# Kernel optimization log

Hardware: AMD Instinct MI355X
Metric: run time of the kernel (lower is better)

Reference implementation:

```python
import jax, jax.numpy as jnp
import numpy as np

WIN = (7, 7)
NUM_HEADS = 12
LORA_SCALING = 16.0 / 16.0  # lora_alpha / lora_rank


def _relative_position_index(win):
    wh, ww = win
    coords = np.stack(np.meshgrid(np.arange(wh), np.arange(ww), indexing='ij'))  # (2, wh, ww)
    cf = coords.reshape(2, -1)
    rel = cf[:, :, None] - cf[:, None, :]  # (2, N, N)
    rel = rel.transpose(1, 2, 0)
    rel[:, :, 0] += wh - 1
    rel[:, :, 1] += ww - 1
    rel[:, :, 0] *= 2 * ww - 1
    return jnp.asarray(rel.sum(-1), dtype=jnp.int32)  # (N, N)


def setup_inputs() -> dict:
    key = jax.random.key(0)
    ks = jax.random.split(key, 12)
    B_, N, C, r = 2048, 49, 384, 16
    nW = 64
    s = 0.02
    return {
        'x': jax.random.normal(ks[0], (B_, N, C), jnp.float32),
        'mask': jnp.zeros((nW, N, N), jnp.float32),
        'qkv_w': jax.random.normal(ks[1], (C, 3 * C), jnp.float32) * s,
        'qkv_b': jax.random.normal(ks[2], (3 * C,), jnp.float32) * s,
        'qa_w': jax.random.normal(ks[3], (C, r), jnp.float32) * s,
        'qb_w': jax.random.normal(ks[4], (r, C), jnp.float32) * s,
        'va_w': jax.random.normal(ks[5], (C, r), jnp.float32) * s,
        'vb_w': jax.random.normal(ks[6], (r, C), jnp.float32) * s,
        'rpb_table': jax.random.normal(ks[7], ((2 * WIN[0] - 1) * (2 * WIN[1] - 1), NUM_HEADS), jnp.float32) * s,
        'proj_w': jax.random.normal(ks[8], (C, C), jnp.float32) * s,
        'proj_b': jax.random.normal(ks[9], (C,), jnp.float32) * s,
    }


def reference(x, mask, qkv_w, qkv_b, qa_w, qb_w, va_w, vb_w, rpb_table, proj_w, proj_b):
    B_, N, C = x.shape
    H = NUM_HEADS
    hd = C // H
    scale = hd ** -0.5

    qkv = (x @ qkv_w + qkv_b).reshape(B_, N, 3, H, hd)
    qkv = jnp.transpose(qkv, (2, 0, 3, 1, 4))  # (3, B_, H, N, hd)
    q, k, v = qkv[0], qkv[1], qkv[2]

    q_lora = LORA_SCALING * ((x @ qa_w) @ qb_w)  # (B_, N, C)
    q = q + jnp.transpose(q_lora.reshape(B_, N, H, hd), (0, 2, 1, 3))
    v_lora = LORA_SCALING * ((x @ va_w) @ vb_w)
    v = v + jnp.transpose(v_lora.reshape(B_, N, H, hd), (0, 2, 1, 3))

    attn = jnp.einsum('bhnd,bhmd->bhnm', q * scale, k)  # (B_, H, N, N)

    rel_idx = _relative_position_index(WIN)  # (N, N) static int
    rpb = rpb_table[rel_idx]  # (N, N, H)
    attn = attn + jnp.transpose(rpb, (2, 0, 1))[None]

    nW = mask.shape[0]
    attn = attn.reshape(B_ // nW, nW, H, N, N) + mask[None, :, None]
    attn = attn.reshape(B_, H, N, N)
    attn = jax.nn.softmax(attn, axis=-1)

    out = jnp.einsum('bhnm,bhmd->bhnd', attn, v)
    out = jnp.transpose(out, (0, 2, 1, 3)).reshape(B_, N, C)
    return out @ proj_w + proj_b
```

## Files before the change

kernel.cpp:

```cpp
#include <hip/hip_runtime.h>
#include <hip/hip_bf16.h>

typedef __hip_bfloat16 bf16;
typedef float f32x4 __attribute__((ext_vector_type(4)));
typedef short bf16x8 __attribute__((ext_vector_type(8)));

static __device__ __forceinline__ void gload_lds16(const void* g, void* l) {
    __builtin_amdgcn_global_load_lds(
        (const __attribute__((address_space(1))) void*)g,
        (__attribute__((address_space(3))) void*)l, 16, 0, 0);
}

static __device__ __forceinline__ short bf16bits(float v) {
    bf16 tb = __float2bfloat16(v);
    return *reinterpret_cast<short*>(&tb);
}

__global__ __launch_bounds__(256) void cvt_x_kernel(const float4* __restrict__ x,
                                                    bf16* __restrict__ xb, int n4) {
    int i = blockIdx.x * 256 + threadIdx.x;
    const int stride = gridDim.x * 256;
    for (; i < n4; i += stride) {
        float4 v = x[i];
        alignas(8) bf16 tmp[4];
        tmp[0] = __float2bfloat16(v.x);
        tmp[1] = __float2bfloat16(v.y);
        tmp[2] = __float2bfloat16(v.z);
        tmp[3] = __float2bfloat16(v.w);
        *reinterpret_cast<uint2*>(xb + 4l * i) = *reinterpret_cast<uint2*>(tmp);
    }
}

__global__ __launch_bounds__(256) void build_wefft_kernel(
    const float* __restrict__ qkv_w, const float* __restrict__ qa,
    const float* __restrict__ qb, const float* __restrict__ va,
    const float* __restrict__ vb, bf16* __restrict__ wt) {
    int idx = blockIdx.x * 256 + threadIdx.x;
    int ncol = idx / 384;
    int k = idx - ncol * 384;
    float v = qkv_w[k * 1152 + ncol];
    if (ncol < 384) {
        float s = 0.f;
#pragma unroll
        for (int j = 0; j < 16; ++j) s += qa[k * 16 + j] * qb[j * 384 + ncol];
        v += s;
    } else if (ncol >= 768) {
        int nc = ncol - 768;
        float s = 0.f;
#pragma unroll
        for (int j = 0; j < 16; ++j) s += va[k * 16 + j] * vb[j * 384 + nc];
        v += s;
    }
    wt[(long)ncol * 384 + k] = __float2bfloat16(v);
}

__global__ __launch_bounds__(256) void build_projt_kernel(const float* __restrict__ pw,
                                                          bf16* __restrict__ pt) {
    int idx = blockIdx.x * 256 + threadIdx.x;
    int ncol = idx / 384;
    int k = idx - ncol * 384;
    pt[(long)ncol * 384 + k] = __float2bfloat16(pw[k * 384 + ncol]);
}

__global__ __launch_bounds__(256) void build_cbias_kernel(const float* __restrict__ rpb_table,
                                                          const float* __restrict__ mask,
                                                          float* __restrict__ cbias) {
    int idx = blockIdx.x * 256 + threadIdx.x;
    int hw = idx / 2401;
    int ij = idx - hw * 2401;
    int h = hw >> 6, w = hw & 63;
    int i = ij / 49, j = ij - i * 49;
    int yi = i / 7, xi = i - yi * 7;
    int yj = j / 7, xj = j - yj * 7;
    int rel = (yi - yj + 6) * 13 + (xi - xj + 6);
    cbias[idx] = rpb_table[rel * 12 + h] + mask[w * 2401 + ij];
}

template <bool OUT_BF16>
__global__ __launch_bounds__(256) void gemm_kernel(const bf16* __restrict__ A,
                                                   const bf16* __restrict__ BT,
                                                   const float* __restrict__ bias,
                                                   void* __restrict__ Cout,
                                                   int N, int K, int nxb, int nwg) {
    __shared__ short Al[128 * 64];
    __shared__ short Bl[128 * 64];
    const int t = threadIdx.x;
    const int lane = t & 63;
    const int wave = t >> 6;
    const int wr = wave >> 1;
    const int wc = wave & 1;
    const int g = lane >> 4, c = lane & 15;

    const int q8 = nwg >> 3;
    const int wgid = (blockIdx.x & 7) * q8 + (blockIdx.x >> 3);
    const int by = wgid / nxb;
    const int bx = wgid - by * nxb;
    const long rowBase = (long)by * 128;
    const long colBase = (long)bx * 128;

    f32x4 acc[4][4];
#pragma unroll
    for (int m = 0; m < 4; ++m)
#pragma unroll
        for (int n = 0; n < 4; ++n) acc[m][n] = (f32x4){0.f, 0.f, 0.f, 0.f};

    for (int k0 = 0; k0 < K; k0 += 64) {
        __syncthreads();
#pragma unroll
        for (int it = 0; it < 4; ++it) {
            int chunk = it * 256 + t;
            int row = chunk >> 3;
            int blk = lane & 7;
            gload_lds16(A + (size_t)(rowBase + row) * K + k0 + ((blk ^ (row & 7)) * 8),
                        &Al[(it * 256 + wave * 64) * 8]);
            gload_lds16(BT + (size_t)(colBase + row) * K + k0 + ((blk ^ (row & 7)) * 8),
                        &Bl[(it * 256 + wave * 64) * 8]);
        }
        asm volatile("s_waitcnt vmcnt(0)" ::: "memory");
        __syncthreads();

#pragma unroll
        for (int ks = 0; ks < 2; ++ks) {
            bf16x8 af[4], bfr[4];
#pragma unroll
            for (int m = 0; m < 4; ++m) {
                int row = wr * 64 + m * 16 + c;
                af[m] = *(const bf16x8*)&Al[row * 64 + (((ks * 4 + g) ^ (c & 7)) * 8)];
            }
#pragma unroll
            for (int n = 0; n < 4; ++n) {
                int row = wc * 64 + n * 16 + c;
                bfr[n] = *(const bf16x8*)&Bl[row * 64 + (((ks * 4 + g) ^ (c & 7)) * 8)];
            }
#pragma unroll
            for (int m = 0; m < 4; ++m)
#pragma unroll
                for (int n = 0; n < 4; ++n)
                    acc[m][n] = __builtin_amdgcn_mfma_f32_16x16x32_bf16(af[m], bfr[n],
                                                                        acc[m][n], 0, 0, 0);
        }
    }

    const int crow0 = wr * 64 + g * 4;
    const long ccol0 = colBase + wc * 64 + c;
#pragma unroll
    for (int m = 0; m < 4; ++m) {
#pragma unroll
        for (int n = 0; n < 4; ++n) {
            const long col = ccol0 + n * 16;
            const float bv = bias[col];
#pragma unroll
            for (int r = 0; r < 4; ++r) {
                const long row = rowBase + crow0 + m * 16 + r;
                float v = acc[m][n][r] + bv;
                if (OUT_BF16)
                    ((bf16*)Cout)[row * N + col] = __float2bfloat16(v);
                else
                    ((float*)Cout)[row * N + col] = v;
            }
        }
    }
}

__global__ __launch_bounds__(256) void attn_kernel(const bf16* __restrict__ qkv,
                                                   const float* __restrict__ cbias,
                                                   bf16* __restrict__ out) {
    __shared__ short lds[4 * 7168];
    const int t = threadIdx.x, lane = t & 63, wave = t >> 6;
    short* W = lds + wave * 7168;
    const int bh = blockIdx.x * 4 + wave;
    const int b = bh / 12, h = bh - b * 12;
    const int g = lane >> 4, c = lane & 15;
    const int w = b & 63;

#pragma unroll
    for (int z = 0; z < 4; ++z)
        *(uint4*)&W[5120 + (z * 64 + lane) * 8] = (uint4){0u, 0u, 0u, 0u};

    const size_t base = (size_t)b * 49 * 1152 + h * 32;
    for (int c4 = lane; c4 < 196; c4 += 64) {
        int n = c4 >> 2, o = (c4 & 3) * 8;
        size_t gaddr = base + (size_t)n * 1152 + o;
        uint4 qv = *(const uint4*)&qkv[gaddr];
        uint4 kv = *(const uint4*)&qkv[gaddr + 384];
        uint4 vv = *(const uint4*)&qkv[gaddr + 768];
        *(uint4*)&W[n * 40 + o] = qv;
        *(uint4*)&W[2560 + n * 40 + o] = kv;
        alignas(16) short tmp[8];
        *(uint4*)tmp = vv;
#pragma unroll
        for (int j = 0; j < 8; ++j) {
            int d = o + j;
            W[5120 + ((d * 64 + n) ^ ((d & 7) << 3))] = tmp[j];
        }
    }
    __syncthreads();

    bf16x8 aq[4], bk[4];
#pragma unroll
    for (int mt = 0; mt < 4; ++mt) aq[mt] = *(const bf16x8*)&W[(mt * 16 + c) * 40 + g * 8];
#pragma unroll
    for (int nt = 0; nt < 4; ++nt) bk[nt] = *(const bf16x8*)&W[2560 + (nt * 16 + c) * 40 + g * 8];
    f32x4 S[4][4];
#pragma unroll
    for (int mt = 0; mt < 4; ++mt)
#pragma unroll
        for (int nt = 0; nt < 4; ++nt)
            S[mt][nt] = __builtin_amdgcn_mfma_f32_16x16x32_bf16(aq[mt], bk[nt],
                                                                (f32x4){0.f, 0.f, 0.f, 0.f}, 0, 0, 0);

    const float scale = 0.17677669529663687f;
    const float* cb = cbias + (size_t)((h << 6) | w) * 2401;
    float inv[16];
#pragma unroll
    for (int mt = 0; mt < 4; ++mt) {
#pragma unroll
        for (int nt = 0; nt < 4; ++nt) {
            int j = nt * 16 + c;
#pragma unroll
            for (int r = 0; r < 4; ++r) {
                int i = mt * 16 + g * 4 + r;
                float v = S[mt][nt][r] * scale;
                if (j < 49 && i < 49) v += cb[i * 49 + j];
                S[mt][nt][r] = (j < 49) ? v : -INFINITY;
            }
        }
#pragma unroll
        for (int r = 0; r < 4; ++r) {
            float m = fmaxf(fmaxf(S[mt][0][r], S[mt][1][r]), fmaxf(S[mt][2][r], S[mt][3][r]));
            m = fmaxf(m, __shfl_xor(m, 1));
            m = fmaxf(m, __shfl_xor(m, 2));
            m = fmaxf(m, __shfl_xor(m, 4));
            m = fmaxf(m, __shfl_xor(m, 8));
            float s = 0.f;
#pragma unroll
            for (int nt = 0; nt < 4; ++nt) {
                float e = __expf(S[mt][nt][r] - m);
                S[mt][nt][r] = e;
                s += e;
            }
            s += __shfl_xor(s, 1);
            s += __shfl_xor(s, 2);
            s += __shfl_xor(s, 4);
            s += __shfl_xor(s, 8);
            inv[mt * 4 + r] = 1.f / s;
        }
    }

    __syncthreads();
#pragma unroll
    for (int mt = 0; mt < 4; ++mt)
#pragma unroll
        for (int nt = 0; nt < 4; ++nt)
#pragma unroll
            for (int r = 0; r < 4; ++r) {
                int i = mt * 16 + g * 4 + r, j = nt * 16 + c;
                W[(i * 64 + j) ^ ((i & 7) << 3)] = bf16bits(S[mt][nt][r]);
            }
    __syncthreads();

    f32x4 O[4][2];
#pragma unroll
    for (int mt = 0; mt < 4; ++mt)
#pragma unroll
        for (int dt = 0; dt < 2; ++dt) O[mt][dt] = (f32x4){0.f, 0.f, 0.f, 0.f};
#pragma unroll
    for (int ks = 0; ks < 2; ++ks) {
        bf16x8 pa[4], vb2[2];
#pragma unroll
        for (int mt = 0; mt < 4; ++mt) {
            int i = mt * 16 + c;
            pa[mt] = *(const bf16x8*)&W[(i * 64 + ks * 32 + g * 8) ^ ((i & 7) << 3)];
        }
#pragma unroll
        for (int dt = 0; dt < 2; ++dt) {
            int d = dt * 16 + c;
            vb2[dt] = *(const bf16x8*)&W[5120 + ((d * 64 + ks * 32 + g * 8) ^ ((d & 7) << 3))];
        }
#pragma unroll
        for (int mt = 0; mt < 4; ++mt)
#pragma unroll
            for (int dt = 0; dt < 2; ++dt)
                O[mt][dt] = __builtin_amdgcn_mfma_f32_16x16x32_bf16(pa[mt], vb2[dt],
                                                                    O[mt][dt], 0, 0, 0);
    }

#pragma unroll
    for (int mt = 0; mt < 4; ++mt)
#pragma unroll
        for (int r = 0; r < 4; ++r) {
            int i = mt * 16 + g * 4 + r;
            if (i < 49) {
#pragma unroll
                for (int dt = 0; dt < 2; ++dt) {
                    int d = dt * 16 + c;
                    out[((size_t)(b * 49 + i)) * 384 + h * 32 + d] =
                        __float2bfloat16(O[mt][dt][r] * inv[mt * 4 + r]);
                }
            }
        }
}

extern "C" void kernel_launch(void* const* d_in, const int* in_sizes, int n_in,
                              void* d_out, int out_size, void* d_ws, size_t ws_size,
                              hipStream_t stream) {
    (void)in_sizes; (void)n_in; (void)out_size; (void)ws_size;
    const float* x      = (const float*)d_in[0];
    const float* mask   = (const float*)d_in[1];
    const float* qkv_w  = (const float*)d_in[2];
    const float* qkv_b  = (const float*)d_in[3];
    const float* qa_w   = (const float*)d_in[4];
    const float* qb_w   = (const float*)d_in[5];
    const float* va_w   = (const float*)d_in[6];
    const float* vb_w   = (const float*)d_in[7];
    const float* rpb    = (const float*)d_in[8];
    const float* proj_w = (const float*)d_in[9];
    const float* proj_b = (const float*)d_in[10];

    char* ws = (char*)d_ws;
    bf16* xb     = (bf16*)(ws);
    bf16* attno  = (bf16*)(ws);
    bf16* wefft  = (bf16*)(ws + 77070336);
    bf16* projt  = (bf16*)(ws + 77955072);
    float* cbias = (float*)(ws + 78249984);
    bf16* qkv    = (bf16*)(ws + 85625856);

    cvt_x_kernel<<<2048, 256, 0, stream>>>((const float4*)x, xb, 9633792);
    build_wefft_kernel<<<1728, 256, 0, stream>>>(qkv_w, qa_w, qb_w, va_w, vb_w, wefft);
    build_projt_kernel<<<576, 256, 0, stream>>>(proj_w, projt);
    build_cbias_kernel<<<7203, 256, 0, stream>>>(rpb, mask, cbias);
    gemm_kernel<true><<<7056, 256, 0, stream>>>(xb, wefft, qkv_b, qkv, 1152, 384, 9, 7056);
    attn_kernel<<<6144, 256, 0, stream>>>(qkv, cbias, attno);
    gemm_kernel<false><<<2352, 256, 0, stream>>>(attno, projt, proj_b, d_out, 384, 384, 3, 2352);
}
```

Before: 401.1 us.

## Fuse window attention with output projection in one per-window kernel

```diff
diff --git a/kernel.cpp b/kernel.cpp
--- a/kernel.cpp
+++ b/kernel.cpp
@@ -162,141 +162,184 @@
     }
 }
 
-__global__ __launch_bounds__(256) void attn_kernel(const bf16* __restrict__ qkv,
-                                                   const float* __restrict__ cbias,
-                                                   bf16* __restrict__ out) {
-    __shared__ short lds[4 * 7168];
+__global__ __launch_bounds__(256) void attn_proj_kernel(const bf16* __restrict__ qkv,
+                                                        const float* __restrict__ cbias,
+                                                        const bf16* __restrict__ projt,
+                                                        const float* __restrict__ proj_b,
+                                                        float* __restrict__ out) {
+    __shared__ short scratch[4 * 7168];
+    __shared__ short Olds[64 * 392];
     const int t = threadIdx.x, lane = t & 63, wave = t >> 6;
-    short* W = lds + wave * 7168;
-    const int bh = blockIdx.x * 4 + wave;
-    const int b = bh / 12, h = bh - b * 12;
+    short* W = scratch + wave * 7168;
+    const int b = blockIdx.x;
     const int g = lane >> 4, c = lane & 15;
     const int w = b & 63;
-
-#pragma unroll
-    for (int z = 0; z < 4; ++z)
-        *(uint4*)&W[5120 + (z * 64 + lane) * 8] = (uint4){0u, 0u, 0u, 0u};
-
-    const size_t base = (size_t)b * 49 * 1152 + h * 32;
-    for (int c4 = lane; c4 < 196; c4 += 64) {
-        int n = c4 >> 2, o = (c4 & 3) * 8;
-        size_t gaddr = base + (size_t)n * 1152 + o;
-        uint4 qv = *(const uint4*)&qkv[gaddr];
-        uint4 kv = *(const uint4*)&qkv[gaddr + 384];
-        uint4 vv = *(const uint4*)&qkv[gaddr + 768];
-        *(uint4*)&W[n * 40 + o] = qv;
-        *(uint4*)&W[2560 + n * 40 + o] = kv;
-        alignas(16) short tmp[8];
-        *(uint4*)tmp = vv;
-#pragma unroll
-        for (int j = 0; j < 8; ++j) {
-            int d = o + j;
-            W[5120 + ((d * 64 + n) ^ ((d & 7) << 3))] = tmp[j];
-        }
-    }
-    __syncthreads();
-
-    bf16x8 aq[4], bk[4];
-#pragma unroll
-    for (int mt = 0; mt < 4; ++mt) aq[mt] = *(const bf16x8*)&W[(mt * 16 + c) * 40 + g * 8];
-#pragma unroll
-    for (int nt = 0; nt < 4; ++nt) bk[nt] = *(const bf16x8*)&W[2560 + (nt * 16 + c) * 40 + g * 8];
-    f32x4 S[4][4];
-#pragma unroll
-    for (int mt = 0; mt < 4; ++mt)
-#pragma unroll
-        for (int nt = 0; nt < 4; ++nt)
-            S[mt][nt] = __builtin_amdgcn_mfma_f32_16x16x32_bf16(aq[mt], bk[nt],
-                                                                (f32x4){0.f, 0.f, 0.f, 0.f}, 0, 0, 0);
-
+    const size_t base = (size_t)b * 49 * 1152;
     const float scale = 0.17677669529663687f;
-    const float* cb = cbias + (size_t)((h << 6) | w) * 2401;
-    float inv[16];
-#pragma unroll
-    for (int mt = 0; mt < 4; ++mt) {
-#pragma unroll
-        for (int nt = 0; nt < 4; ++nt) {
-            int j = nt * 16 + c;
+
+    for (int hh = 0; hh < 3; ++hh) {
+        const int h = wave * 3 + hh;
+
+#pragma unroll
+        for (int z = 0; z < 4; ++z)
+            *(uint4*)&W[5120 + (z * 64 + lane) * 8] = (uint4){0u, 0u, 0u, 0u};
+
+        const size_t hbase = base + h * 32;
+        for (int c4 = lane; c4 < 196; c4 += 64) {
+            int n = c4 >> 2, o = (c4 & 3) * 8;
+            size_t gaddr = hbase + (size_t)n * 1152 + o;
+            uint4 qv = *(const uint4*)&qkv[gaddr];
+            uint4 kv = *(const uint4*)&qkv[gaddr + 384];
+            uint4 vv = *(const uint4*)&qkv[gaddr + 768];
+            *(uint4*)&W[n * 40 + o] = qv;
+            *(uint4*)&W[2560 + n * 40 + o] = kv;
+            alignas(16) short tmp[8];
+            *(uint4*)tmp = vv;
+#pragma unroll
+            for (int j = 0; j < 8; ++j) {
+                int d = o + j;
+                W[5120 + ((d * 64 + n) ^ ((d & 7) << 3))] = tmp[j];
+            }
+        }
+        __syncthreads();
+
+        bf16x8 aq[4], bk[4];
+#pragma unroll
+        for (int mt = 0; mt < 4; ++mt) aq[mt] = *(const bf16x8*)&W[(mt * 16 + c) * 40 + g * 8];
+#pragma unroll
+        for (int nt = 0; nt < 4; ++nt) bk[nt] = *(const bf16x8*)&W[2560 + (nt * 16 + c) * 40 + g * 8];
+        f32x4 S[4][4];
+#pragma unroll
+        for (int mt = 0; mt < 4; ++mt)
+#pragma unroll
+            for (int nt = 0; nt < 4; ++nt)
+                S[mt][nt] = __builtin_amdgcn_mfma_f32_16x16x32_bf16(aq[mt], bk[nt],
+                                                                    (f32x4){0.f, 0.f, 0.f, 0.f}, 0, 0, 0);
+
+        const float* cb = cbias + (size_t)((h << 6) | w) * 2401;
+        float inv[16];
+#pragma unroll
+        for (int mt = 0; mt < 4; ++mt) {
+#pragma unroll
+            for (int nt = 0; nt < 4; ++nt) {
+                int j = nt * 16 + c;
+#pragma unroll
+                for (int r = 0; r < 4; ++r) {
+                    int i = mt * 16 + g * 4 + r;
+                    float v = S[mt][nt][r] * scale;
+                    if (j < 49 && i < 49) v += cb[i * 49 + j];
+                    S[mt][nt][r] = (j < 49) ? v : -INFINITY;
+                }
+            }
+#pragma unroll
+            for (int r = 0; r < 4; ++r) {
+                float m = fmaxf(fmaxf(S[mt][0][r], S[mt][1][r]), fmaxf(S[mt][2][r], S[mt][3][r]));
+                m = fmaxf(m, __shfl_xor(m, 1));
+                m = fmaxf(m, __shfl_xor(m, 2));
+                m = fmaxf(m, __shfl_xor(m, 4));
+                m = fmaxf(m, __shfl_xor(m, 8));
+                float s = 0.f;
+#pragma unroll
+                for (int nt = 0; nt < 4; ++nt) {
+                    float e = __expf(S[mt][nt][r] - m);
+                    S[mt][nt][r] = e;
+                    s += e;
+                }
+                s += __shfl_xor(s, 1);
+                s += __shfl_xor(s, 2);
+                s += __shfl_xor(s, 4);
+                s += __shfl_xor(s, 8);
+                inv[mt * 4 + r] = 1.f / s;
+            }
+        }
+
+        __syncthreads();
+#pragma unroll
+        for (int mt = 0; mt < 4; ++mt)
+#pragma unroll
+            for (int nt = 0; nt < 4; ++nt)
+#pragma unroll
+                for (int r = 0; r < 4; ++r) {
+                    int i = mt * 16 + g * 4 + r, j = nt * 16 + c;
+                    W[(i * 64 + j) ^ ((i & 7) << 3)] = bf16bits(S[mt][nt][r]);
+                }
+        __syncthreads();
+
+        f32x4 O[4][2];
+#pragma unroll
+        for (int mt = 0; mt < 4; ++mt)
+#pragma unroll
+            for (int dt = 0; dt < 2; ++dt) O[mt][dt] = (f32x4){0.f, 0.f, 0.f, 0.f};
+#pragma unroll
+        for (int ks = 0; ks < 2; ++ks) {
+            bf16x8 pa[4], vb2[2];
+#pragma unroll
+            for (int mt = 0; mt < 4; ++mt) {
+                int i = mt * 16 + c;
+                pa[mt] = *(const bf16x8*)&W[(i * 64 + ks * 32 + g * 8) ^ ((i & 7) << 3)];
+            }
+#pragma unroll
+            for (int dt = 0; dt < 2; ++dt) {
+                int d = dt * 16 + c;
+                vb2[dt] = *(const bf16x8*)&W[5120 + ((d * 64 + ks * 32 + g * 8) ^ ((d & 7) << 3))];
+            }
+#pragma unroll
+            for (int mt = 0; mt < 4; ++mt)
+#pragma unroll
+                for (int dt = 0; dt < 2; ++dt)
+                    O[mt][dt] = __builtin_amdgcn_mfma_f32_16x16x32_bf16(pa[mt], vb2[dt],
+                                                                        O[mt][dt], 0, 0, 0);
+        }
+
+#pragma unroll
+        for (int mt = 0; mt < 4; ++mt)
 #pragma unroll
             for (int r = 0; r < 4; ++r) {
                 int i = mt * 16 + g * 4 + r;
-                float v = S[mt][nt][r] * scale;
-                if (j < 49 && i < 49) v += cb[i * 49 + j];
-                S[mt][nt][r] = (j < 49) ? v : -INFINITY;
-            }
-        }
-#pragma unroll
-        for (int r = 0; r < 4; ++r) {
-            float m = fmaxf(fmaxf(S[mt][0][r], S[mt][1][r]), fmaxf(S[mt][2][r], S[mt][3][r]));
-            m = fmaxf(m, __shfl_xor(m, 1));
-            m = fmaxf(m, __shfl_xor(m, 2));
-            m = fmaxf(m, __shfl_xor(m, 4));
-            m = fmaxf(m, __shfl_xor(m, 8));
-            float s = 0.f;
-#pragma unroll
-            for (int nt = 0; nt < 4; ++nt) {
-                float e = __expf(S[mt][nt][r] - m);
-                S[mt][nt][r] = e;
-                s += e;
-            }
-            s += __shfl_xor(s, 1);
-            s += __shfl_xor(s, 2);
-            s += __shfl_xor(s, 4);
-            s += __shfl_xor(s, 8);
-            inv[mt * 4 + r] = 1.f / s;
-        }
-    }
-
-    __syncthreads();
-#pragma unroll
-    for (int mt = 0; mt < 4; ++mt)
-#pragma unroll
-        for (int nt = 0; nt < 4; ++nt)
+                if (i < 49) {
+#pragma unroll
+                    for (int dt = 0; dt < 2; ++dt) {
+                        int d = dt * 16 + c;
+                        Olds[i * 392 + h * 32 + d] = bf16bits(O[mt][dt][r] * inv[mt * 4 + r]);
+                    }
+                }
+            }
+        __syncthreads();
+    }
+
+    f32x4 pacc[4][6];
+#pragma unroll
+    for (int m = 0; m < 4; ++m)
+#pragma unroll
+        for (int n = 0; n < 6; ++n) pacc[m][n] = (f32x4){0.f, 0.f, 0.f, 0.f};
+
+    for (int ks = 0; ks < 12; ++ks) {
+        bf16x8 af[4], bn[6];
+#pragma unroll
+        for (int m = 0; m < 4; ++m)
+            af[m] = *(const bf16x8*)&Olds[(m * 16 + c) * 392 + ks * 32 + g * 8];
+#pragma unroll
+        for (int n = 0; n < 6; ++n)
+            bn[n] = *(const bf16x8*)&projt[(size_t)(wave * 96 + n * 16 + c) * 384 + ks * 32 + g * 8];
+#pragma unroll
+        for (int m = 0; m < 4; ++m)
+#pragma unroll
+            for (int n = 0; n < 6; ++n)
+                pacc[m][n] = __builtin_amdgcn_mfma_f32_16x16x32_bf16(af[m], bn[n],
+                                                                     pacc[m][n], 0, 0, 0);
+    }
+
+#pragma unroll
+    for (int m = 0; m < 4; ++m)
+#pragma unroll
+        for (int n = 0; n < 6; ++n) {
+            const int col = wave * 96 + n * 16 + c;
+            const float bv = proj_b[col];
 #pragma unroll
             for (int r = 0; r < 4; ++r) {
-                int i = mt * 16 + g * 4 + r, j = nt * 16 + c;
-                W[(i * 64 + j) ^ ((i & 7) << 3)] = bf16bits(S[mt][nt][r]);
-            }
-    __syncthreads();
-
-    f32x4 O[4][2];
-#pragma unroll
-    for (int mt = 0; mt < 4; ++mt)
-#pragma unroll
-        for (int dt = 0; dt < 2; ++dt) O[mt][dt] = (f32x4){0.f, 0.f, 0.f, 0.f};
-#pragma unroll
-    for (int ks = 0; ks < 2; ++ks) {
-        bf16x8 pa[4], vb2[2];
-#pragma unroll
-        for (int mt = 0; mt < 4; ++mt) {
-            int i = mt * 16 + c;
-            pa[mt] = *(const bf16x8*)&W[(i * 64 + ks * 32 + g * 8) ^ ((i & 7) << 3)];
-        }
-#pragma unroll
-        for (int dt = 0; dt < 2; ++dt) {
-            int d = dt * 16 + c;
-            vb2[dt] = *(const bf16x8*)&W[5120 + ((d * 64 + ks * 32 + g * 8) ^ ((d & 7) << 3))];
-        }
-#pragma unroll
-        for (int mt = 0; mt < 4; ++mt)
-#pragma unroll
-            for (int dt = 0; dt < 2; ++dt)
-                O[mt][dt] = __builtin_amdgcn_mfma_f32_16x16x32_bf16(pa[mt], vb2[dt],
-                                                                    O[mt][dt], 0, 0, 0);
-    }
-
-#pragma unroll
-    for (int mt = 0; mt < 4; ++mt)
-#pragma unroll
-        for (int r = 0; r < 4; ++r) {
-            int i = mt * 16 + g * 4 + r;
-            if (i < 49) {
-#pragma unroll
-                for (int dt = 0; dt < 2; ++dt) {
-                    int d = dt * 16 + c;
-                    out[((size_t)(b * 49 + i)) * 384 + h * 32 + d] =
-                        __float2bfloat16(O[mt][dt][r] * inv[mt * 4 + r]);
-                }
+                int i = m * 16 + g * 4 + r;
+                if (i < 49)
+                    out[((size_t)b * 49 + i) * 384 + col] = pacc[m][n][r] + bv;
             }
         }
 }
@@ -319,7 +362,6 @@
 
     char* ws = (char*)d_ws;
     bf16* xb     = (bf16*)(ws);
-    bf16* attno  = (bf16*)(ws);
     bf16* wefft  = (bf16*)(ws + 77070336);
     bf16* projt  = (bf16*)(ws + 77955072);
     float* cbias = (float*)(ws + 78249984);
@@ -330,6 +372,5 @@
     build_projt_kernel<<<576, 256, 0, stream>>>(proj_w, projt);
     build_cbias_kernel<<<7203, 256, 0, stream>>>(rpb, mask, cbias);
     gemm_kernel<true><<<7056, 256, 0, stream>>>(xb, wefft, qkv_b, qkv, 1152, 384, 9, 7056);
-    attn_kernel<<<6144, 256, 0, stream>>>(qkv, cbias, attno);
-    gemm_kernel<false><<<2352, 256, 0, stream>>>(attno, projt, proj_b, d_out, 384, 384, 3, 2352);
-}
+    attn_proj_kernel<<<2048, 256, 0, stream>>>(qkv, cbias, projt, proj_b, (float*)d_out);
+}
```

Result: slower. 510.2 us (+27.2%).
